# Kernel optimization log

Hardware: AMD Instinct MI355X
Metric: run time of the kernel (lower is better)

Reference implementation:

```python
import jax, jax.numpy as jnp
import numpy as np

K = 3          # kernel size
STRIDE = 1
PAD = 1
DIL = 1
K2 = K * K     # number of sampling locations per output pixel


def conv2d(x, w, b, stride=STRIDE, pad=PAD, dil=DIL):
    # x: [B,C,H,W], w: [O,I,K,K], b: [O]
    out = jax.lax.conv_general_dilated(
        x, w, window_strides=(stride, stride),
        padding=[(pad, pad), (pad, pad)], rhs_dilation=(dil, dil),
        dimension_numbers=('NCHW', 'OIHW', 'NCHW'))
    return out + b[None, :, None, None]


def bilinear_sample(x, sy, sx):
    # x: [B,C,H,W]; sy, sx: [B,K2,Ho,Wo] float sampling coords (y, x)
    # zero padding outside the image (torchvision deform_conv2d semantics)
    B, C, H, W = x.shape
    x_flat = x.reshape(B, C, H * W)

    y0 = jnp.floor(sy)
    x0 = jnp.floor(sx)
    wy1 = sy - y0  # frac weights
    wx1 = sx - x0
    wy0 = 1.0 - wy1
    wx0 = 1.0 - wx1

    def gather(yi, xi):
        valid = ((yi >= 0) & (yi < H) & (xi >= 0) & (xi < W)).astype(x.dtype)
        yc = jnp.clip(yi, 0, H - 1).astype(jnp.int32)
        xc = jnp.clip(xi, 0, W - 1).astype(jnp.int32)
        idx = (yc * W + xc).reshape(B, 1, -1)  # [B,1,K2*Ho*Wo]
        v = jnp.take_along_axis(x_flat, idx, axis=2)  # [B,C,K2*Ho*Wo]
        v = v.reshape(B, C, *yi.shape[1:])            # [B,C,K2,Ho,Wo]
        return v * valid[:, None]

    out = (gather(y0,     x0    ) * (wy0 * wx0)[:, None]
         + gather(y0,     x0 + 1) * (wy0 * wx1)[:, None]
         + gather(y0 + 1, x0    ) * (wy1 * wx0)[:, None]
         + gather(y0 + 1, x0 + 1) * (wy1 * wx1)[:, None])
    return out  # [B,C,K2,Ho,Wo]


def setup_inputs() -> dict:
    key = jax.random.key(0)
    ks = jax.random.split(key, 6)
    B, C, H, W = 4, 64, 128, 128
    Cout = 64
    x = jax.random.normal(ks[0], (B, C, H, W), jnp.float32)
    # offset conv: 2*K2 output channels; small init -> small offsets (realistic)
    w_off = jax.random.normal(ks[1], (2 * K2, C, K, K), jnp.float32) * 0.01
    b_off = jnp.zeros((2 * K2,), jnp.float32)
    # mask conv: K2 output channels, sigmoid activation
    w_mask = jax.random.normal(ks[2], (K2, C, K, K), jnp.float32) * 0.01
    b_mask = jnp.zeros((K2,), jnp.float32)  # mask_init_bias = 0
    # main deformable conv weights
    w = jax.random.normal(ks[3], (Cout, C, K, K), jnp.float32) * (1.0 / np.sqrt(C * K2))
    b = jnp.zeros((Cout,), jnp.float32)
    return {"x": x, "w_off": w_off, "b_off": b_off,
            "w_mask": w_mask, "b_mask": b_mask, "w": w, "b": b}


def reference(x, w_off, b_off, w_mask, b_mask, w, b):
    B, C, H, W = x.shape
    Cout = w.shape[0]

    offset = conv2d(x, w_off, b_off)                    # [B,2*K2,Ho,Wo]
    mask = jax.nn.sigmoid(conv2d(x, w_mask, b_mask))    # [B,K2,Ho,Wo]
    Ho, Wo = offset.shape[2], offset.shape[3]

    off = offset.reshape(B, K2, 2, Ho, Wo)
    dy, dx = off[:, :, 0], off[:, :, 1]                 # torchvision layout: (y,x) pairs

    ki = (jnp.arange(K2) // K).astype(jnp.float32)      # kernel row index
    kj = (jnp.arange(K2) % K).astype(jnp.float32)       # kernel col index
    base_y = (jnp.arange(Ho, dtype=jnp.float32) * STRIDE - PAD)[None, :, None] \
             + (ki * DIL)[:, None, None]                # [K2,Ho,1]
    base_x = (jnp.arange(Wo, dtype=jnp.float32) * STRIDE - PAD)[None, None, :] \
             + (kj * DIL)[:, None, None]                # [K2,1,Wo]

    sy = base_y[None] + dy                              # [B,K2,Ho,Wo]
    sx = base_x[None] + dx

    sampled = bilinear_sample(x, sy, sx) * mask[:, None]  # [B,C,K2,Ho,Wo]
    out = jnp.einsum('bckhw,ock->bohw', sampled, w.reshape(Cout, C, K2))
    return out + b[None, :, None, None]
```

## Files before the change

kernel.cpp:

```cpp
#include <hip/hip_runtime.h>
#include <math.h>

typedef __attribute__((ext_vector_type(8))) short short8;
typedef __attribute__((ext_vector_type(4))) float f32x4;
typedef unsigned short ushort_t;
typedef unsigned int uint_t;

#define HH 128
#define WW 128
#define CC 64
#define HWp 16384

__device__ inline ushort_t f2bf(float f) {
    uint_t u = __float_as_uint(f);
    uint_t r = (u + 0x7FFFu + ((u >> 16) & 1u)) >> 16;
    return (ushort_t)r;
}
__device__ inline float blo(uint_t u) { return __uint_as_float(u << 16); }
__device__ inline float bhi(uint_t u) { return __uint_as_float(u & 0xFFFF0000u); }
__device__ inline short8 bc8(uint4 v) { return __builtin_bit_cast(short8, v); }

__device__ inline uint_t pk2(f32x4 wv, uint_t a, uint_t b, uint_t c, uint_t d) {
    float lo = wv.x * blo(a) + wv.y * blo(b) + wv.z * blo(c) + wv.w * blo(d);
    float hi = wv.x * bhi(a) + wv.y * bhi(b) + wv.z * bhi(c) + wv.w * bhi(d);
    uint_t r;
    asm("v_cvt_pk_bf16_f32 %0, %1, %2" : "=v"(r) : "v"(lo), "v"(hi));
    return r;
}
__device__ inline short8 bilerp8(f32x4 wv, uint4 A, uint4 B, uint4 C, uint4 D) {
    uint4 r;
    r.x = pk2(wv, A.x, B.x, C.x, D.x);
    r.y = pk2(wv, A.y, B.y, C.y, D.y);
    r.z = pk2(wv, A.z, B.z, C.z, D.z);
    r.w = pk2(wv, A.w, B.w, C.w, D.w);
    return __builtin_bit_cast(short8, r);
}

__global__ __launch_bounds__(256) void k_prep(const float* __restrict__ x,
        ushort_t* __restrict__ xtb,
        const float* __restrict__ w_off, const float* __restrict__ w_mask,
        const float* __restrict__ w,
        ushort_t* __restrict__ wpom, ushort_t* __restrict__ wpm) {
    __shared__ __align__(16) float tile[64][68];
    int bid = blockIdx.x;
    int t = threadIdx.x;
    if (bid < 1024) {
        int xs = (bid & 1) * 64;
        int y  = (bid >> 1) & 127;
        int b  = bid >> 8;
#pragma unroll
        for (int i = 0; i < 4; ++i) {
            int c  = i * 16 + (t >> 4);
            int xl = (t & 15) << 2;
            float4 v = *(const float4*)&x[(((size_t)b * CC + c) * HH + y) * WW + xs + xl];
            *(float4*)&tile[c][xl] = v;
        }
        __syncthreads();
#pragma unroll
        for (int i = 0; i < 8; ++i) {
            int pxl = i * 8 + (t >> 5);
            int cp  = t & 31;
            float v0 = tile[cp * 2][pxl], v1 = tile[cp * 2 + 1][pxl];
            uint_t pk;
            asm("v_cvt_pk_bf16_f32 %0, %1, %2" : "=v"(pk) : "v"(v0), "v"(v1));
            *(uint_t*)&xtb[(((size_t)b * HH + y) * WW + xs + pxl) * CC + cp * 2] = pk;
        }
    } else {
        int idx = (bid - 1024) * 256 + t;
        if (idx < 18432) {
            int e = idx;
            int j = e & 7, l = (e >> 3) & 63, mf = (e >> 9) & 1, ks = e >> 10;
            int ch = mf * 16 + (l & 15);
            int k = ks * 32 + ((l >> 4) << 3) + j;
            int c = k & 63, kk = k >> 6;
            float v = 0.f;
            if (ch < 18) v = w_off[(ch * CC + c) * 9 + kk];
            else if (ch < 27) v = w_mask[((ch - 18) * CC + c) * 9 + kk];
            wpom[idx] = f2bf(v);
        } else if (idx < 18432 + 36864) {
            int e = idx - 18432;
            int j = e & 7, l = (e >> 3) & 63, mf = (e >> 9) & 3, ks = e >> 11;
            int o = mf * 16 + (l & 15);
            int k = ks * 32 + ((l >> 4) << 3) + j;
            int c = k & 63, kk = k >> 6;
            wpm[e] = f2bf(w[(o * CC + c) * 9 + kk]);
        }
    }
}

__global__ __launch_bounds__(256, 4) void k_conv_om(const ushort_t* __restrict__ xtb,
        const uint4* __restrict__ wpom, const float* __restrict__ b_off,
        const float* __restrict__ b_mask, float* __restrict__ om) {
    __shared__ ushort_t xrow[3 * 68 * 64];
    int blk = blockIdx.x;
    int b = blk >> 8, rem = blk & 255;
    int y = rem >> 1, xh = (rem & 1) * 64;
    int t = threadIdx.x;

    for (int ky = 0; ky < 3; ++ky) {
        int yy = y + ky - 1;
        bool rok = (yy >= 0) && (yy < HH);
#pragma unroll
        for (int i = 0; i < 3; ++i) {
            int t2 = i * 256 + t;
            if (t2 < 528) {
                int cl = t2 >> 3;
                int c0 = (t2 & 7) * 8;
                int xcoord = xh - 1 + cl;
                bool ok = rok && (xcoord >= 0) && (xcoord < WW);
                uint4 v = make_uint4(0u, 0u, 0u, 0u);
                if (ok) v = *(const uint4*)&xtb[(((size_t)b * HWp) + yy * WW + xcoord) * CC + c0];
                int idx = ((ky * 68 + cl) * 64 + c0) ^ ((cl & 7) << 3);
                *(uint4*)&xrow[idx] = v;
            }
        }
    }
    __syncthreads();

    int lane = t & 63, w = t >> 6;
    int lm = lane & 15, lg = lane >> 4;
    int pxl = w * 16 + lm;
    f32x4 acc[2] = {};
#pragma unroll
    for (int ks = 0; ks < 18; ++ks) {
        int kk = ks >> 1;
        int kyy = kk / 3, kxx = kk % 3;
        int c0 = (ks & 1) * 32 + lg * 8;
        short8 a0 = bc8(wpom[(ks * 2 + 0) * 64 + lane]);
        short8 a1 = bc8(wpom[(ks * 2 + 1) * 64 + lane]);
        int cl = pxl + kxx;
        int idx = ((kyy * 68 + cl) * 64 + c0) ^ ((cl & 7) << 3);
        short8 bf = *(const short8*)&xrow[idx];
        acc[0] = __builtin_amdgcn_mfma_f32_16x16x32_bf16(a0, bf, acc[0], 0, 0, 0);
        acc[1] = __builtin_amdgcn_mfma_f32_16x16x32_bf16(a1, bf, acc[1], 0, 0, 0);
    }
    int px = xh + pxl;
#pragma unroll
    for (int mf = 0; mf < 2; ++mf)
#pragma unroll
        for (int r = 0; r < 4; ++r) {
            int ch = mf * 16 + lg * 4 + r;
            if (ch < 27) {
                float v = acc[mf][r] + (ch < 18 ? b_off[ch] : b_mask[ch - 18]);
                if (ch >= 18) v = 1.f / (1.f + __expf(-v));
                om[(((size_t)b * 27 + ch) << 14) + (y << 7) + px] = v;
            }
        }
}

__global__ __launch_bounds__(512, 6) void k_fused(const ushort_t* __restrict__ xtb,
        const float* __restrict__ om, const uint4* __restrict__ wpm,
        const float* __restrict__ bias, float* __restrict__ out) {
    __shared__ __align__(16) ushort_t sm[32 * 576];
    __shared__ __align__(16) float prm[288 * 8];
    int blk = blockIdx.x;
    int b = blk >> 9, rem = blk & 511;
    int y = rem >> 2, xs = (rem & 3) * 32;
    int t = threadIdx.x, lane = t & 63, w = t >> 6;
    const char* xbB = (const char*)xtb + ((size_t)b << 21);
    const float* omb = om + (((size_t)b * 27) << 14) + (y << 7) + xs;
    float* wprm = prm + w * (36 * 8);

    if (lane < 36) {
        int pxl = lane / 9, k = lane - pxl * 9;
        int px = (w << 2) + pxl;
        int ki = k / 3, kj = k - ki * 3;
        int x = xs + px;
        float dy = omb[((2 * k) << 14) + px];
        float dx = omb[((2 * k + 1) << 14) + px];
        float m  = omb[((18 + k) << 14) + px];
        float sy = (float)(y - 1 + ki) + dy;
        float sx = (float)(x - 1 + kj) + dx;
        float fy = floorf(sy), fx = floorf(sx);
        float wy1 = sy - fy, wx1 = sx - fx;
        float wy0 = 1.f - wy1, wx0 = 1.f - wx1;
        int iy0 = (int)fy, ix0 = (int)fx;
        int iy1 = iy0 + 1, ix1 = ix0 + 1;
        bool vy0 = (iy0 >= 0) & (iy0 < HH);
        bool vy1 = (iy1 >= 0) & (iy1 < HH);
        float wyr0 = vy0 ? wy0 : (vy1 ? wy1 : 0.f);
        int   ry0  = vy0 ? iy0 : (vy1 ? iy1 : 0);
        float wyr1 = (vy0 & vy1) ? wy1 : 0.f;
        int   ry1  = min(max(iy1, 0), HH - 1);
        int bx = min(max(ix0, 0), WW - 2);
        float wxh0 = (bx == ix0) ? wx0 : ((bx == ix1) ? wx1 : 0.f);
        float wxh1 = (bx + 1 == ix1) ? wx1 : ((bx + 1 == ix0) ? wx0 : 0.f);
        f32x4 wv4 = { m * wyr0 * wxh0, m * wyr0 * wxh1,
                      m * wyr1 * wxh0, m * wyr1 * wxh1 };
        f32x4 aux;
        aux.x = __uint_as_float((uint_t)(((ry0 << 7) + bx) << 7));
        aux.y = __uint_as_float((uint_t)(((ry1 << 7) + bx) << 7));
        aux.z = __uint_as_float((uint_t)(px * 576 + k * 64));
        aux.w = __uint_as_float((uint_t)(((px ^ k) & 7) << 3));
        float* pp = wprm + lane * 8;
        *(f32x4*)pp = wv4;
        *(f32x4*)(pp + 4) = aux;
    }
    asm volatile("s_waitcnt lgkmcnt(0)" ::: "memory");
    __builtin_amdgcn_sched_barrier(0);

    {
        int g = lane >> 3, j = lane & 7;
        uint_t j16 = (uint_t)(j << 4);
        uint_t jw  = (uint_t)(j << 3);
        uint4 axv[5];
#pragma unroll
        for (int r = 0; r < 5; ++r) {
            int sl = g + r * 8; sl = sl > 35 ? 35 : sl;
            axv[r] = *(const uint4*)(wprm + sl * 8 + 4);
        }
        uint4 tlA, trA, blA, brA, tlB, trB, blB, brB;
        {
            uint_t aT = axv[0].x + j16, aB = axv[0].y + j16;
            tlA = *(const uint4*)(xbB + aT);  trA = *(const uint4*)(xbB + aT + 128);
            blA = *(const uint4*)(xbB + aB);  brA = *(const uint4*)(xbB + aB + 128);
        }
#pragma unroll
        for (int r = 0; r < 5; ++r) {
            if (r < 4) {
                uint_t aT = axv[r + 1].x + j16, aB = axv[r + 1].y + j16;
                tlB = *(const uint4*)(xbB + aT);  trB = *(const uint4*)(xbB + aT + 128);
                blB = *(const uint4*)(xbB + aB);  brB = *(const uint4*)(xbB + aB + 128);
            }
            int sl = g + r * 8; sl = sl > 35 ? 35 : sl;
            f32x4 wv = *(const f32x4*)(wprm + sl * 8);
            short8 bf = bilerp8(wv, tlA, trA, blA, brA);
            if (r < 4 || g < 4) {
                uint_t widx = (axv[r].z + jw) ^ axv[r].w;
                *(short8*)&sm[widx] = bf;
            }
            tlA = tlB; trA = trB; blA = blB; brA = brB;
        }
    }
    __syncthreads();

    int lm = lane & 15, lg = lane >> 4;
    int mf = w & 3, nh = w >> 2;
    int px_r = (nh << 4) + lm;
    f32x4 acc = {};
#pragma unroll
    for (int ks = 0; ks < 18; ++ks) {
        short8 af = bc8(wpm[((ks << 2) + mf) * 64 + lane]);
        int bidx = (px_r * 576 + (ks << 5) + (lg << 3)) ^ (((px_r ^ (ks >> 1)) & 7) << 3);
        short8 bf = *(const short8*)&sm[bidx];
        acc = __builtin_amdgcn_mfma_f32_16x16x32_bf16(af, bf, acc, 0, 0, 0);
    }
#pragma unroll
    for (int r = 0; r < 4; ++r) {
        int o = (mf << 4) + (lg << 2) + r;
        out[(((size_t)b * 64 + o) << 14) + (y << 7) + xs + px_r] = acc[r] + bias[o];
    }
}

extern "C" void kernel_launch(void* const* d_in, const int* in_sizes, int n_in,
                              void* d_out, int out_size, void* d_ws, size_t ws_size,
                              hipStream_t stream) {
    const float* x      = (const float*)d_in[0];
    const float* w_off  = (const float*)d_in[1];
    const float* b_off  = (const float*)d_in[2];
    const float* w_mask = (const float*)d_in[3];
    const float* b_mask = (const float*)d_in[4];
    const float* w      = (const float*)d_in[5];
    const float* bias   = (const float*)d_in[6];
    float* out = (float*)d_out;

    char* ws = (char*)d_ws;
    ushort_t* xtb  = (ushort_t*)(ws);
    float*    om   = (float*)(ws + 8388608);
    ushort_t* wpom = (ushort_t*)(ws + 15466496);
    ushort_t* wpm  = (ushort_t*)(ws + 15503360);

    hipLaunchKernelGGL(k_prep, dim3(1240), dim3(256), 0, stream,
                       x, xtb, w_off, w_mask, w, wpom, wpm);
    hipLaunchKernelGGL(k_conv_om, dim3(1024), dim3(256), 0, stream,
                       xtb, (const uint4*)wpom, b_off, b_mask, om);
    hipLaunchKernelGGL(k_fused, dim3(2048), dim3(512), 0, stream,
                       xtb, om, (const uint4*)wpm, bias, out);
}
```

Before: 50.60 us.

## Fuse offset/mask convolution into deformable conv kernel via shared-memory tile

Drops the separate offset/mask conv kernel. Each fused block now loads a 3-row x 34-column x-halo into shared memory, computes the 27 offset/mask channels with MFMA on 4 waves, and keeps them in a shared tile instead of a global buffer. The same shared buffer is then reused for the bilinear-sampled patch. This removes one launch and the global write and read of the offset/mask tensor. In exchange it adds an extra sync phase and halo load per block, and half the waves sit idle during the offset conv.

```diff
diff --git a/kernel.cpp b/kernel.cpp
--- a/kernel.cpp
+++ b/kernel.cpp
@@ -88,87 +88,71 @@
     }
 }
 
-__global__ __launch_bounds__(256, 4) void k_conv_om(const ushort_t* __restrict__ xtb,
-        const uint4* __restrict__ wpom, const float* __restrict__ b_off,
-        const float* __restrict__ b_mask, float* __restrict__ om) {
-    __shared__ ushort_t xrow[3 * 68 * 64];
-    int blk = blockIdx.x;
-    int b = blk >> 8, rem = blk & 255;
-    int y = rem >> 1, xh = (rem & 1) * 64;
-    int t = threadIdx.x;
-
-    for (int ky = 0; ky < 3; ++ky) {
-        int yy = y + ky - 1;
-        bool rok = (yy >= 0) && (yy < HH);
-#pragma unroll
-        for (int i = 0; i < 3; ++i) {
-            int t2 = i * 256 + t;
-            if (t2 < 528) {
-                int cl = t2 >> 3;
-                int c0 = (t2 & 7) * 8;
-                int xcoord = xh - 1 + cl;
-                bool ok = rok && (xcoord >= 0) && (xcoord < WW);
-                uint4 v = make_uint4(0u, 0u, 0u, 0u);
-                if (ok) v = *(const uint4*)&xtb[(((size_t)b * HWp) + yy * WW + xcoord) * CC + c0];
-                int idx = ((ky * 68 + cl) * 64 + c0) ^ ((cl & 7) << 3);
-                *(uint4*)&xrow[idx] = v;
-            }
-        }
-    }
-    __syncthreads();
-
-    int lane = t & 63, w = t >> 6;
-    int lm = lane & 15, lg = lane >> 4;
-    int pxl = w * 16 + lm;
-    f32x4 acc[2] = {};
-#pragma unroll
-    for (int ks = 0; ks < 18; ++ks) {
-        int kk = ks >> 1;
-        int kyy = kk / 3, kxx = kk % 3;
-        int c0 = (ks & 1) * 32 + lg * 8;
-        short8 a0 = bc8(wpom[(ks * 2 + 0) * 64 + lane]);
-        short8 a1 = bc8(wpom[(ks * 2 + 1) * 64 + lane]);
-        int cl = pxl + kxx;
-        int idx = ((kyy * 68 + cl) * 64 + c0) ^ ((cl & 7) << 3);
-        short8 bf = *(const short8*)&xrow[idx];
-        acc[0] = __builtin_amdgcn_mfma_f32_16x16x32_bf16(a0, bf, acc[0], 0, 0, 0);
-        acc[1] = __builtin_amdgcn_mfma_f32_16x16x32_bf16(a1, bf, acc[1], 0, 0, 0);
-    }
-    int px = xh + pxl;
-#pragma unroll
-    for (int mf = 0; mf < 2; ++mf)
-#pragma unroll
-        for (int r = 0; r < 4; ++r) {
-            int ch = mf * 16 + lg * 4 + r;
-            if (ch < 27) {
-                float v = acc[mf][r] + (ch < 18 ? b_off[ch] : b_mask[ch - 18]);
-                if (ch >= 18) v = 1.f / (1.f + __expf(-v));
-                om[(((size_t)b * 27 + ch) << 14) + (y << 7) + px] = v;
-            }
-        }
-}
-
 __global__ __launch_bounds__(512, 6) void k_fused(const ushort_t* __restrict__ xtb,
-        const float* __restrict__ om, const uint4* __restrict__ wpm,
+        const uint4* __restrict__ wpom, const uint4* __restrict__ wpm,
+        const float* __restrict__ b_off, const float* __restrict__ b_mask,
         const float* __restrict__ bias, float* __restrict__ out) {
-    __shared__ __align__(16) ushort_t sm[32 * 576];
+    __shared__ __align__(16) ushort_t smx[32 * 576];
+    __shared__ __align__(16) float om_tile[32 * 28];
     __shared__ __align__(16) float prm[288 * 8];
     int blk = blockIdx.x;
     int b = blk >> 9, rem = blk & 511;
     int y = rem >> 2, xs = (rem & 3) * 32;
     int t = threadIdx.x, lane = t & 63, w = t >> 6;
     const char* xbB = (const char*)xtb + ((size_t)b << 21);
-    const float* omb = om + (((size_t)b * 27) << 14) + (y << 7) + xs;
     float* wprm = prm + w * (36 * 8);
+
+    for (int i = t; i < 816; i += 512) {
+        int ky = i / 272;
+        int r2 = i - ky * 272;
+        int cl = r2 >> 3, cj = r2 & 7;
+        int yy = y + ky - 1;
+        int xc = xs - 1 + cl;
+        bool ok = (yy >= 0) && (yy < HH) && (xc >= 0) && (xc < WW);
+        uint4 v = make_uint4(0u, 0u, 0u, 0u);
+        if (ok) v = *(const uint4*)&xtb[((size_t)b * HWp + yy * WW + xc) * CC + cj * 8];
+        int idx = ((ky * 36 + cl) * 64 + cj * 8) ^ ((cl & 7) << 3);
+        *(uint4*)&smx[idx] = v;
+    }
+    __syncthreads();
+
+    if (w < 4) {
+        int mfc = w & 1, nfc = w >> 1;
+        int lm = lane & 15, lg = lane >> 4;
+        f32x4 acc = {};
+#pragma unroll
+        for (int ks = 0; ks < 18; ++ks) {
+            int kk = ks >> 1;
+            int kyy = kk / 3, kxx = kk % 3;
+            int c0 = (ks & 1) * 32 + lg * 8;
+            short8 af = bc8(wpom[(ks * 2 + mfc) * 64 + lane]);
+            int cl = nfc * 16 + lm + kxx;
+            int idx = ((kyy * 36 + cl) * 64 + c0) ^ ((cl & 7) << 3);
+            short8 bf = *(const short8*)&smx[idx];
+            acc = __builtin_amdgcn_mfma_f32_16x16x32_bf16(af, bf, acc, 0, 0, 0);
+        }
+        int px = nfc * 16 + lm;
+#pragma unroll
+        for (int r = 0; r < 4; ++r) {
+            int ch = mfc * 16 + lg * 4 + r;
+            if (ch < 27) {
+                float v = acc[r] + (ch < 18 ? b_off[ch] : b_mask[ch - 18]);
+                if (ch >= 18) v = 1.f / (1.f + __expf(-v));
+                om_tile[px * 28 + ch] = v;
+            }
+        }
+    }
+    __syncthreads();
 
     if (lane < 36) {
         int pxl = lane / 9, k = lane - pxl * 9;
         int px = (w << 2) + pxl;
         int ki = k / 3, kj = k - ki * 3;
         int x = xs + px;
-        float dy = omb[((2 * k) << 14) + px];
-        float dx = omb[((2 * k + 1) << 14) + px];
-        float m  = omb[((18 + k) << 14) + px];
+        const float* omp = om_tile + px * 28;
+        float dy = omp[2 * k];
+        float dx = omp[2 * k + 1];
+        float m  = omp[18 + k];
         float sy = (float)(y - 1 + ki) + dy;
         float sx = (float)(x - 1 + kj) + dx;
         float fy = floorf(sy), fx = floorf(sx);
@@ -227,7 +211,7 @@
             short8 bf = bilerp8(wv, tlA, trA, blA, brA);
             if (r < 4 || g < 4) {
                 uint_t widx = (axv[r].z + jw) ^ axv[r].w;
-                *(short8*)&sm[widx] = bf;
+                *(short8*)&smx[widx] = bf;
             }
             tlA = tlB; trA = trB; blA = blB; brA = brB;
         }
@@ -242,7 +226,7 @@
     for (int ks = 0; ks < 18; ++ks) {
         short8 af = bc8(wpm[((ks << 2) + mf) * 64 + lane]);
         int bidx = (px_r * 576 + (ks << 5) + (lg << 3)) ^ (((px_r ^ (ks >> 1)) & 7) << 3);
-        short8 bf = *(const short8*)&sm[bidx];
+        short8 bf = *(const short8*)&smx[bidx];
         acc = __builtin_amdgcn_mfma_f32_16x16x32_bf16(af, bf, acc, 0, 0, 0);
     }
 #pragma unroll
@@ -266,14 +250,12 @@
 
     char* ws = (char*)d_ws;
     ushort_t* xtb  = (ushort_t*)(ws);
-    float*    om   = (float*)(ws + 8388608);
-    ushort_t* wpom = (ushort_t*)(ws + 15466496);
-    ushort_t* wpm  = (ushort_t*)(ws + 15503360);
+    ushort_t* wpom = (ushort_t*)(ws + 8388608);
+    ushort_t* wpm  = (ushort_t*)(ws + 8425472);
 
     hipLaunchKernelGGL(k_prep, dim3(1240), dim3(256), 0, stream,
                        x, xtb, w_off, w_mask, w, wpom, wpm);
-    hipLaunchKernelGGL(k_conv_om, dim3(1024), dim3(256), 0, stream,
-                       xtb, (const uint4*)wpom, b_off, b_mask, om);
     hipLaunchKernelGGL(k_fused, dim3(2048), dim3(512), 0, stream,
-                       xtb, om, (const uint4*)wpm, bias, out);
-}
+                       xtb, (const uint4*)wpom, (const uint4*)wpm,
+                       b_off, b_mask, bias, out);
+}
```

Result: slower. 52.21 us (+3.2%).

## Tile offset/mask buffer per 16-pixel group and shrink fused blocks to 16 pixels

Applied to the files above, without the earlier changes.

The offset/mask conv now writes its output in a tiled layout, one 432-float block per (batch,row,16-pixel group), so the fused kernel reads contiguous parameters instead of strided planes. The fused kernel drops from 32 to 16 pixels per block with 256 threads and 4096 blocks, and each wave covers one 16-output-channel tile. The per-sample bilinear parameters are passed between lanes with wave shuffles rather than through a shared-memory staging buffer, which removes that LDS traffic and its wait. Smaller blocks raise occupancy and halve shared memory per block, at the cost of more blocks and more total weight-fragment loads.

```diff
diff --git a/kernel.cpp b/kernel.cpp
--- a/kernel.cpp
+++ b/kernel.cpp
@@ -88,7 +88,7 @@
     }
 }
 
-__global__ __launch_bounds__(256, 4) void k_conv_om(const ushort_t* __restrict__ xtb,
+__global__ __launch_bounds__(256, 6) void k_conv_om(const ushort_t* __restrict__ xtb,
         const uint4* __restrict__ wpom, const float* __restrict__ b_off,
         const float* __restrict__ b_mask, float* __restrict__ om) {
     __shared__ ushort_t xrow[3 * 68 * 64];
@@ -134,7 +134,8 @@
         acc[0] = __builtin_amdgcn_mfma_f32_16x16x32_bf16(a0, bf, acc[0], 0, 0, 0);
         acc[1] = __builtin_amdgcn_mfma_f32_16x16x32_bf16(a1, bf, acc[1], 0, 0, 0);
     }
-    int px = xh + pxl;
+    int xg = (xh >> 4) + w;
+    size_t tb = ((size_t)((b * 128 + y) * 8 + xg)) * 432;
 #pragma unroll
     for (int mf = 0; mf < 2; ++mf)
 #pragma unroll
@@ -143,32 +144,32 @@
             if (ch < 27) {
                 float v = acc[mf][r] + (ch < 18 ? b_off[ch] : b_mask[ch - 18]);
                 if (ch >= 18) v = 1.f / (1.f + __expf(-v));
-                om[(((size_t)b * 27 + ch) << 14) + (y << 7) + px] = v;
-            }
-        }
-}
-
-__global__ __launch_bounds__(512, 6) void k_fused(const ushort_t* __restrict__ xtb,
-        const float* __restrict__ om, const uint4* __restrict__ wpm,
+                om[tb + ch * 16 + lm] = v;
+            }
+        }
+}
+
+__global__ __launch_bounds__(256, 8) void k_fused(const ushort_t* __restrict__ xtb,
+        const float* __restrict__ omt, const uint4* __restrict__ wpm,
         const float* __restrict__ bias, float* __restrict__ out) {
-    __shared__ __align__(16) ushort_t sm[32 * 576];
-    __shared__ __align__(16) float prm[288 * 8];
+    __shared__ __align__(16) ushort_t sm[16 * 576];
     int blk = blockIdx.x;
-    int b = blk >> 9, rem = blk & 511;
-    int y = rem >> 2, xs = (rem & 3) * 32;
+    int b = blk >> 10, rem = blk & 1023;
+    int y = rem >> 3, xg = rem & 7, xs = xg << 4;
     int t = threadIdx.x, lane = t & 63, w = t >> 6;
     const char* xbB = (const char*)xtb + ((size_t)b << 21);
-    const float* omb = om + (((size_t)b * 27) << 14) + (y << 7) + xs;
-    float* wprm = prm + w * (36 * 8);
-
+    const float* omb = omt + ((size_t)((b * 128 + y) * 8 + xg)) * 432;
+
+    float pw0 = 0.f, pw1 = 0.f, pw2 = 0.f, pw3 = 0.f;
+    int paT = 0, paB = 0, ppk = 0;
     if (lane < 36) {
         int pxl = lane / 9, k = lane - pxl * 9;
-        int px = (w << 2) + pxl;
+        int px_t = (w << 2) + pxl;
         int ki = k / 3, kj = k - ki * 3;
-        int x = xs + px;
-        float dy = omb[((2 * k) << 14) + px];
-        float dx = omb[((2 * k + 1) << 14) + px];
-        float m  = omb[((18 + k) << 14) + px];
+        int x = xs + px_t;
+        float dy = omb[32 * k + px_t];
+        float dx = omb[32 * k + 16 + px_t];
+        float m  = omb[288 + 16 * k + px_t];
         float sy = (float)(y - 1 + ki) + dy;
         float sx = (float)(x - 1 + kj) + dx;
         float fy = floorf(sy), fx = floorf(sx);
@@ -185,70 +186,73 @@
         int bx = min(max(ix0, 0), WW - 2);
         float wxh0 = (bx == ix0) ? wx0 : ((bx == ix1) ? wx1 : 0.f);
         float wxh1 = (bx + 1 == ix1) ? wx1 : ((bx + 1 == ix0) ? wx0 : 0.f);
-        f32x4 wv4 = { m * wyr0 * wxh0, m * wyr0 * wxh1,
-                      m * wyr1 * wxh0, m * wyr1 * wxh1 };
-        f32x4 aux;
-        aux.x = __uint_as_float((uint_t)(((ry0 << 7) + bx) << 7));
-        aux.y = __uint_as_float((uint_t)(((ry1 << 7) + bx) << 7));
-        aux.z = __uint_as_float((uint_t)(px * 576 + k * 64));
-        aux.w = __uint_as_float((uint_t)(((px ^ k) & 7) << 3));
-        float* pp = wprm + lane * 8;
-        *(f32x4*)pp = wv4;
-        *(f32x4*)(pp + 4) = aux;
-    }
-    asm volatile("s_waitcnt lgkmcnt(0)" ::: "memory");
-    __builtin_amdgcn_sched_barrier(0);
+        pw0 = m * wyr0 * wxh0;
+        pw1 = m * wyr0 * wxh1;
+        pw2 = m * wyr1 * wxh0;
+        pw3 = m * wyr1 * wxh1;
+        paT = (int)((uint_t)(((ry0 << 7) + bx) << 7));
+        paB = (int)((uint_t)(((ry1 << 7) + bx) << 7));
+        ppk = (int)((uint_t)(px_t * 576 + k * 64) |
+                    ((uint_t)(((px_t ^ k) & 7) << 3) << 16));
+    }
 
     {
         int g = lane >> 3, j = lane & 7;
         uint_t j16 = (uint_t)(j << 4);
         uint_t jw  = (uint_t)(j << 3);
-        uint4 axv[5];
+        int slA = g;
+        float wA0 = __shfl(pw0, slA), wA1 = __shfl(pw1, slA);
+        float wA2 = __shfl(pw2, slA), wA3 = __shfl(pw3, slA);
+        uint_t aTA = (uint_t)__shfl(paT, slA) + j16;
+        uint_t aBA = (uint_t)__shfl(paB, slA) + j16;
+        uint_t pkA = (uint_t)__shfl(ppk, slA);
+        uint4 tlA = *(const uint4*)(xbB + aTA);
+        uint4 trA = *(const uint4*)(xbB + aTA + 128);
+        uint4 blA = *(const uint4*)(xbB + aBA);
+        uint4 brA = *(const uint4*)(xbB + aBA + 128);
 #pragma unroll
         for (int r = 0; r < 5; ++r) {
-            int sl = g + r * 8; sl = sl > 35 ? 35 : sl;
-            axv[r] = *(const uint4*)(wprm + sl * 8 + 4);
-        }
-        uint4 tlA, trA, blA, brA, tlB, trB, blB, brB;
-        {
-            uint_t aT = axv[0].x + j16, aB = axv[0].y + j16;
-            tlA = *(const uint4*)(xbB + aT);  trA = *(const uint4*)(xbB + aT + 128);
-            blA = *(const uint4*)(xbB + aB);  brA = *(const uint4*)(xbB + aB + 128);
-        }
-#pragma unroll
-        for (int r = 0; r < 5; ++r) {
+            float wB0, wB1, wB2, wB3;
+            uint_t pkB = 0;
+            uint4 tlB, trB, blB, brB;
             if (r < 4) {
-                uint_t aT = axv[r + 1].x + j16, aB = axv[r + 1].y + j16;
-                tlB = *(const uint4*)(xbB + aT);  trB = *(const uint4*)(xbB + aT + 128);
-                blB = *(const uint4*)(xbB + aB);  brB = *(const uint4*)(xbB + aB + 128);
-            }
-            int sl = g + r * 8; sl = sl > 35 ? 35 : sl;
-            f32x4 wv = *(const f32x4*)(wprm + sl * 8);
+                int slB = g + (r + 1) * 8; slB = slB > 35 ? 35 : slB;
+                wB0 = __shfl(pw0, slB); wB1 = __shfl(pw1, slB);
+                wB2 = __shfl(pw2, slB); wB3 = __shfl(pw3, slB);
+                uint_t aTB = (uint_t)__shfl(paT, slB) + j16;
+                uint_t aBB = (uint_t)__shfl(paB, slB) + j16;
+                pkB = (uint_t)__shfl(ppk, slB);
+                tlB = *(const uint4*)(xbB + aTB);
+                trB = *(const uint4*)(xbB + aTB + 128);
+                blB = *(const uint4*)(xbB + aBB);
+                brB = *(const uint4*)(xbB + aBB + 128);
+            }
+            f32x4 wv = { wA0, wA1, wA2, wA3 };
             short8 bf = bilerp8(wv, tlA, trA, blA, brA);
             if (r < 4 || g < 4) {
-                uint_t widx = (axv[r].z + jw) ^ axv[r].w;
+                uint_t widx = ((pkA & 0xFFFFu) + jw) ^ (pkA >> 16);
                 *(short8*)&sm[widx] = bf;
             }
+            wA0 = wB0; wA1 = wB1; wA2 = wB2; wA3 = wB3;
+            pkA = pkB;
             tlA = tlB; trA = trB; blA = blB; brA = brB;
         }
     }
     __syncthreads();
 
     int lm = lane & 15, lg = lane >> 4;
-    int mf = w & 3, nh = w >> 2;
-    int px_r = (nh << 4) + lm;
     f32x4 acc = {};
 #pragma unroll
     for (int ks = 0; ks < 18; ++ks) {
-        short8 af = bc8(wpm[((ks << 2) + mf) * 64 + lane]);
-        int bidx = (px_r * 576 + (ks << 5) + (lg << 3)) ^ (((px_r ^ (ks >> 1)) & 7) << 3);
+        short8 af = bc8(wpm[((ks << 2) + w) * 64 + lane]);
+        int bidx = (lm * 576 + (ks << 5) + (lg << 3)) ^ (((lm ^ (ks >> 1)) & 7) << 3);
         short8 bf = *(const short8*)&sm[bidx];
         acc = __builtin_amdgcn_mfma_f32_16x16x32_bf16(af, bf, acc, 0, 0, 0);
     }
 #pragma unroll
     for (int r = 0; r < 4; ++r) {
-        int o = (mf << 4) + (lg << 2) + r;
-        out[(((size_t)b * 64 + o) << 14) + (y << 7) + xs + px_r] = acc[r] + bias[o];
+        int o = (w << 4) + (lg << 2) + r;
+        out[(((size_t)b * 64 + o) << 14) + (y << 7) + xs + lm] = acc[r] + bias[o];
     }
 }
 
@@ -274,6 +278,6 @@
                        x, xtb, w_off, w_mask, w, wpom, wpm);
     hipLaunchKernelGGL(k_conv_om, dim3(1024), dim3(256), 0, stream,
                        xtb, (const uint4*)wpom, b_off, b_mask, om);
-    hipLaunchKernelGGL(k_fused, dim3(2048), dim3(512), 0, stream,
+    hipLaunchKernelGGL(k_fused, dim3(4096), dim3(256), 0, stream,
                        xtb, om, (const uint4*)wpm, bias, out);
 }
```

Measured after the change: 49.15 us. -2.9%, faster.
